# Kernel optimization log

Measured on AMD Instinct MI355X. Metric: run time of the kernel, lower is better.

Reference implementation:

```python
import jax, jax.numpy as jnp
import numpy as np

B, N, T, ET = 256, 256, 100, 4
MSG_HID, MSG_OUT, N_HID, N_CLASSES = 128, 64, 64, 2
N_EDGES = N * (N - 1) // 2  # 32640


def _xavier(k, out_dim, in_dim):
    std = (2.0 / (in_dim + out_dim)) ** 0.5
    return jax.random.normal(k, (out_dim, in_dim), dtype=jnp.float32) * std


def setup_inputs() -> dict:
    key = jax.random.key(0)
    ks = jax.random.split(key, 7)
    return {
        "inputs": jax.random.normal(ks[0], (B, N, T), dtype=jnp.float32),
        "sparse_edges": jax.random.uniform(ks[1], (B, N_EDGES, ET), dtype=jnp.float32),
        "w1": _xavier(ks[2], MSG_HID, N), "b1": jnp.full((MSG_HID,), 0.1, jnp.float32),
        "w2": _xavier(ks[3], MSG_OUT, MSG_HID), "b2": jnp.full((MSG_OUT,), 0.1, jnp.float32),
        "wo1": _xavier(ks[4], N_HID, MSG_OUT), "bo1": jnp.full((N_HID,), 0.1, jnp.float32),
        "wo2": _xavier(ks[5], N_HID, N_HID), "bo2": jnp.full((N_HID,), 0.1, jnp.float32),
        "wo3": _xavier(ks[6], N_CLASSES, N_HID), "bo3": jnp.full((N_CLASSES,), 0.1, jnp.float32),
    }


def reference(inputs, sparse_edges, w1, b1, w2, b2, wo1, bo1, wo2, bo2, wo3, bo3):
    b, n, _ = inputs.shape
    r, c = np.triu_indices(n, k=1)  # static index pattern
    # Scatter all non-null edge types at once: [B, ET-1, N, N]
    se = jnp.swapaxes(sparse_edges[:, :, 1:], 1, 2)  # [B, ET-1, E]
    adj = jnp.zeros((b, se.shape[1], n, n), dtype=se.dtype)
    adj = adj.at[:, :, r, c].set(se)
    adj = adj + jnp.swapaxes(adj, -1, -2)  # symmetrize
    # Message MLP (dropout_prob = 0 -> identity)
    h = jax.nn.relu(jnp.einsum('beij,hj->beih', adj, w1) + b1)   # [B,ET-1,N,msg_hid]
    m = jax.nn.relu(jnp.einsum('beih,oh->beio', h, w2) + b2)     # [B,ET-1,N,msg_out]
    # Weighted sum over edge types: weight for type i is i*0.2, i=1..ET-1
    wts = (jnp.arange(1, sparse_edges.shape[2]) * 0.2).astype(m.dtype)
    out = jnp.einsum('beio,e->bio', m, wts)                      # [B,N,msg_out]
    # Output head
    p = jax.nn.relu(out @ wo1.T + bo1)
    p = jax.nn.relu(p @ wo2.T + bo2)
    p = jnp.mean(p, axis=1)  # mean over atoms
    return p @ wo3.T + bo3   # [B, n_classes]
```

## Files before the change

### kernel.cpp

```cpp
#include <hip/hip_runtime.h>

#define E_ 32640

typedef __bf16 bf16x8 __attribute__((ext_vector_type(8)));
typedef float f32x4 __attribute__((ext_vector_type(4)));

__device__ __forceinline__ unsigned short cvt1(float f) {
  return __builtin_bit_cast(unsigned short, (__bf16)f);
}

__device__ __forceinline__ bf16x8 ldfrag(const unsigned short* base, int row, int kbyte, int rowbytes) {
  int byte = (row * rowbytes + kbyte) ^ ((row & 7) << 4);
  return *reinterpret_cast<const bf16x8*>(reinterpret_cast<const char*>(base) + byte);
}
__device__ __forceinline__ void st2(unsigned short* base, int row, int colbyte, int rowbytes, unsigned short v) {
  int byte = (row * rowbytes + colbyte) ^ ((row & 7) << 4);
  *reinterpret_cast<unsigned short*>(reinterpret_cast<char*>(base) + byte) = v;
}
__device__ __forceinline__ void stA3(unsigned short* sA0, int lr, int cb, float4 v) {
  int byte = (lr * 512 + cb) ^ ((lr & 7) << 4);
  char* p = reinterpret_cast<char*>(sA0) + byte;
  *reinterpret_cast<unsigned short*>(p)         = cvt1(v.y);
  *reinterpret_cast<unsigned short*>(p + 8192)  = cvt1(v.z);
  *reinterpret_cast<unsigned short*>(p + 16384) = cvt1(v.w);
}
__device__ __forceinline__ bf16x8 pack8(float4 lo, float4 hi) {
  bf16x8 r;
  r[0] = (__bf16)lo.x; r[1] = (__bf16)lo.y; r[2] = (__bf16)lo.z; r[3] = (__bf16)lo.w;
  r[4] = (__bf16)hi.x; r[5] = (__bf16)hi.y; r[6] = (__bf16)hi.z; r[7] = (__bf16)hi.w;
  return r;
}

__device__ __forceinline__ int ubase(int i) { return (i * (511 - i)) >> 1; }

__device__ __forceinline__ void decode_g(int g, int& gi, int& j) {
  float disc = (float)(261121 - 8 * g);
  int t = (int)((511.0f - sqrtf(disc)) * 0.5f);
  while (t * (511 - t) > 2 * g) --t;
  while ((t + 1) * (510 - t) <= 2 * g) ++t;
  gi = t;
  j = g - ((t * (511 - t)) >> 1) + t + 1;
}

__device__ __forceinline__ void stage_lower(const float4* seB, unsigned short* sA,
                                            int r0, int glane, int ngroups) {
  const int sub = glane >> 4, l16 = glane & 15;
  const int nStrips = r0 + 15;
  for (int j0 = sub; j0 < nStrips; j0 += ngroups * 4) {
    float4 v[4]; int lr[4], cb[4]; bool ok[4];
    #pragma unroll
    for (int kk = 0; kk < 4; ++kk) {
      int j  = j0 + kk * ngroups;
      int i0 = (j + 1 > r0) ? (j + 1) : r0;
      int cnt = r0 + 16 - i0;
      int ii = i0 + l16;
      bool val = (j < nStrips) && (l16 < cnt);
      int u = j * 255 - ((j * (j - 1)) >> 1) + (ii - j - 1);
      ok[kk] = val; lr[kk] = ii - r0; cb[kk] = j * 2;
      v[kk] = seB[val ? u : 0];
    }
    #pragma unroll
    for (int kk = 0; kk < 4; ++kk)
      if (ok[kk]) stA3(sA, lr[kk], cb[kk], v[kk]);
  }
}

__device__ __forceinline__ void stage_upper_sync(const float4* seB, unsigned short* sA,
                                                 int r0, int tid) {
  const int s0 = ubase(r0);
  const int S  = ubase(r0 + 16) - s0;
  int t = tid;
  float4 p0 = {}, p1 = {};
  if (t < S)       p0 = seB[s0 + t];
  if (t + 512 < S) p1 = seB[s0 + t + 512];
  for (; t < S; t += 512) {
    float4 v = p0; p0 = p1;
    if (t + 1024 < S) p1 = seB[s0 + t + 1024];
    int gi, j; decode_g(s0 + t, gi, j);
    stA3(sA, gi - r0, j * 2, v);
  }
}

__global__ __launch_bounds__(512, 2) void chunk_kernel(
    const float* __restrict__ se_g,
    const float* __restrict__ w1,  const float* __restrict__ b1,
    const float* __restrict__ w2,  const float* __restrict__ b2,
    const float* __restrict__ wo1, const float* __restrict__ bo1,
    const float* __restrict__ wo2, const float* __restrict__ bo2,
    float* __restrict__ ws)
{
  __shared__ __align__(16) unsigned short sA[3 * 16 * 256];
  __shared__ __align__(16) unsigned short sH3[3 * 16 * 128];
  __shared__ __align__(16) unsigned short sXP[2 * 16 * 64];
  __shared__ float sAccC[64];

  const int tid = threadIdx.x;
  const int i   = blockIdx.x;
  const int half  = i >> 8;
  const int within = i & 255;
  const int batch = (within & 7) * 32 + (within >> 3);
  const int cbase = half * 8;

  const int w   = tid >> 6;
  const int l   = tid & 63;
  const int l15 = l & 15;
  const int lk  = l >> 4;
  const int kb0 = lk * 16;

  const int c1 = w;
  const int c2 = w & 3;
  const bool isHead = (w < 4);

  if (tid < 64) sAccC[tid] = 0.f;

  bf16x8 W1f[8];
  {
    const float* p = w1 + (c1 * 16 + l15) * 256 + lk * 8;
    #pragma unroll
    for (int ks = 0; ks < 8; ++ks)
      W1f[ks] = pack8(*reinterpret_cast<const float4*>(p + ks * 32),
                      *reinterpret_cast<const float4*>(p + ks * 32 + 4));
  }
  bf16x8 W2f[4];
  {
    const float* p = w2 + (c2 * 16 + l15) * 128 + lk * 8;
    #pragma unroll
    for (int ks = 0; ks < 4; ++ks)
      W2f[ks] = pack8(*reinterpret_cast<const float4*>(p + ks * 32),
                      *reinterpret_cast<const float4*>(p + ks * 32 + 4));
  }
  const float b1v  = b1[c1 * 16 + l15];
  const float b2v  = b2[c2 * 16 + l15];
  const float bo1v = bo1[c2 * 16 + l15];
  const float bo2v = bo2[c2 * 16 + l15];

  const float4* seB = reinterpret_cast<const float4*>(se_g) + (size_t)batch * E_;
  unsigned short* sX = sXP;
  unsigned short* sP = sXP + 16 * 64;

  {
    int r0 = cbase * 16;
    stage_upper_sync(seB, sA, r0, tid);
    stage_lower(seB, sA, r0, tid, 32);
    if (tid < 16) {
      int byte = (tid * 512 + (r0 + tid) * 2) ^ ((tid & 7) << 4);
      char* p = reinterpret_cast<char*>(sA) + byte;
      *reinterpret_cast<unsigned short*>(p)         = 0;
      *reinterpret_cast<unsigned short*>(p + 8192)  = 0;
      *reinterpret_cast<unsigned short*>(p + 16384) = 0;
    }
  }
  __syncthreads();

  for (int cc = 0; cc < 8; ++cc) {
    const int r0 = (cbase + cc) * 16;
    const bool more = (cc < 7);
    const int nr0 = r0 + 16;

    float4 pf[8];
    int s0 = 0, S = 0;
    if (more) {
      s0 = ubase(nr0);
      S  = ubase(nr0 + 16) - s0;
      #pragma unroll
      for (int k = 0; k < 8; ++k) {
        int t = tid + k * 512;
        pf[k] = seB[s0 + (t < S ? t : 0)];
      }
    }

    {
      const int ccol = c1 * 16 + l15;
      #pragma unroll
      for (int e = 0; e < 3; ++e) {
        f32x4 acc = {0, 0, 0, 0};
        const unsigned short* sAe = sA + e * 4096;
        #pragma unroll
        for (int ks = 0; ks < 8; ++ks)
          acc = __builtin_amdgcn_mfma_f32_16x16x32_bf16(
              ldfrag(sAe, l15, ks * 64 + kb0, 512), W1f[ks], acc, 0, 0, 0);
        unsigned short* sHe = sH3 + e * 2048;
        #pragma unroll
        for (int r = 0; r < 4; ++r)
          st2(sHe, lk * 4 + r, ccol * 2, 256, cvt1(fmaxf(acc[r] + b1v, 0.f)));
      }
    }
    __syncthreads();

    if (more) {
      #pragma unroll
      for (int k = 0; k < 8; ++k) {
        int t = tid + k * 512;
        if (t < S) {
          int gi, j; decode_g(s0 + t, gi, j);
          stA3(sA, gi - nr0, j * 2, pf[k]);
        }
      }
      if (tid < 16) {
        int byte = (tid * 512 + (nr0 + tid) * 2) ^ ((tid & 7) << 4);
        char* p = reinterpret_cast<char*>(sA) + byte;
        *reinterpret_cast<unsigned short*>(p)         = 0;
        *reinterpret_cast<unsigned short*>(p + 8192)  = 0;
        *reinterpret_cast<unsigned short*>(p + 16384) = 0;
      }
    }
    bf16x8 WO1f[2], WO2f[2];
    if (isHead) {
      const float* q1 = wo1 + (c2 * 16 + l15) * 64 + lk * 8;
      const float* q2 = wo2 + (c2 * 16 + l15) * 64 + lk * 8;
      float4 wa0 = *reinterpret_cast<const float4*>(q1);
      float4 wa1 = *reinterpret_cast<const float4*>(q1 + 4);
      float4 wa2 = *reinterpret_cast<const float4*>(q1 + 32);
      float4 wa3 = *reinterpret_cast<const float4*>(q1 + 36);
      float4 wb0 = *reinterpret_cast<const float4*>(q2);
      float4 wb1 = *reinterpret_cast<const float4*>(q2 + 4);
      float4 wb2 = *reinterpret_cast<const float4*>(q2 + 32);
      float4 wb3 = *reinterpret_cast<const float4*>(q2 + 36);
      f32x4 outAcc = {0, 0, 0, 0};
      #pragma unroll
      for (int e = 0; e < 3; ++e) {
        f32x4 acc = {0, 0, 0, 0};
        const unsigned short* sHe = sH3 + e * 2048;
        #pragma unroll
        for (int ks = 0; ks < 4; ++ks)
          acc = __builtin_amdgcn_mfma_f32_16x16x32_bf16(
              ldfrag(sHe, l15, ks * 64 + kb0, 256), W2f[ks], acc, 0, 0, 0);
        float wte = 0.2f * (float)(e + 1);
        #pragma unroll
        for (int r = 0; r < 4; ++r)
          outAcc[r] += wte * fmaxf(acc[r] + b2v, 0.f);
      }
      WO1f[0] = pack8(wa0, wa1); WO1f[1] = pack8(wa2, wa3);
      WO2f[0] = pack8(wb0, wb1); WO2f[1] = pack8(wb2, wb3);
      #pragma unroll
      for (int r = 0; r < 4; ++r)
        st2(sX, lk * 4 + r, (c2 * 16 + l15) * 2, 128, cvt1(outAcc[r]));
    } else if (more) {
      stage_lower(seB, sA, nr0, tid - 256, 16);
    }
    __syncthreads();

    if (isHead) {
      f32x4 acc = {0, 0, 0, 0};
      #pragma unroll
      for (int ks = 0; ks < 2; ++ks)
        acc = __builtin_amdgcn_mfma_f32_16x16x32_bf16(
            ldfrag(sX, l15, ks * 64 + kb0, 128), WO1f[ks], acc, 0, 0, 0);
      #pragma unroll
      for (int r = 0; r < 4; ++r)
        st2(sP, lk * 4 + r, (c2 * 16 + l15) * 2, 128, cvt1(fmaxf(acc[r] + bo1v, 0.f)));
    }
    __syncthreads();

    if (isHead) {
      f32x4 acc = {0, 0, 0, 0};
      #pragma unroll
      for (int ks = 0; ks < 2; ++ks)
        acc = __builtin_amdgcn_mfma_f32_16x16x32_bf16(
            ldfrag(sP, l15, ks * 64 + kb0, 128), WO2f[ks], acc, 0, 0, 0);
      float s = 0.f;
      #pragma unroll
      for (int r = 0; r < 4; ++r) s += fmaxf(acc[r] + bo2v, 0.f);
      s += __shfl_xor(s, 16);
      s += __shfl_xor(s, 32);
      if (lk == 0) sAccC[c2 * 16 + l15] += s;
    }
    __syncthreads();
  }

  if (tid < 64) ws[((size_t)batch * 2 + half) * 64 + tid] = sAccC[tid];
}

__global__ __launch_bounds__(512) void finish_kernel(
    const float* __restrict__ ws,
    const float* __restrict__ wo3, const float* __restrict__ bo3,
    float* __restrict__ out)
{
  int b = blockIdx.x * 8 + (threadIdx.x >> 6);
  int l = threadIdx.x & 63;
  float s = (ws[((size_t)b * 2 + 0) * 64 + l] + ws[((size_t)b * 2 + 1) * 64 + l]) * (1.0f / 256.0f);
  float v0 = s * wo3[l];
  float v1 = s * wo3[64 + l];
  #pragma unroll
  for (int off = 32; off > 0; off >>= 1) {
    v0 += __shfl_down(v0, off);
    v1 += __shfl_down(v1, off);
  }
  if (l == 0) {
    out[b * 2 + 0] = v0 + bo3[0];
    out[b * 2 + 1] = v1 + bo3[1];
  }
}

extern "C" void kernel_launch(void* const* d_in, const int* in_sizes, int n_in,
                              void* d_out, int out_size, void* d_ws, size_t ws_size,
                              hipStream_t stream) {
  (void)in_sizes; (void)n_in; (void)ws_size; (void)out_size;
  const float* se  = (const float*)d_in[1];
  const float* w1  = (const float*)d_in[2];
  const float* b1  = (const float*)d_in[3];
  const float* w2  = (const float*)d_in[4];
  const float* b2  = (const float*)d_in[5];
  const float* wo1 = (const float*)d_in[6];
  const float* bo1 = (const float*)d_in[7];
  const float* wo2 = (const float*)d_in[8];
  const float* bo2 = (const float*)d_in[9];
  const float* wo3 = (const float*)d_in[10];
  const float* bo3 = (const float*)d_in[11];
  float* ws = (float*)d_ws;
  chunk_kernel<<<dim3(512), dim3(512), 0, stream>>>(
      se, w1, b1, w2, b2, wo1, bo1, wo2, bo2, ws);
  finish_kernel<<<dim3(32), dim3(512), 0, stream>>>(ws, wo3, bo3, (float*)d_out);
}
```

Baseline: 103.8 us.

## Split into densify pass writing bf16 adjacency to workspace, then async-DMA GEMM kernel

Adds a densify kernel that scatters the sparse edge list into dense bf16 adjacency planes in global workspace. A separate GEMM kernel then streams 32-row tiles through double-buffered LDS via global_load_lds. It processes 32 rows per MFMA pass and keeps all head weights in registers. The aim is to take the irregular scatter and triangular index decoding off the MFMA critical path and to overlap loads with compute. The cost is about 100MB of extra global write and read traffic plus an extra launch. The old fused kernel stays as a fallback when the workspace is too small.

```diff
diff --git a/kernel.cpp b/kernel.cpp
--- a/kernel.cpp
+++ b/kernel.cpp
@@ -1,6 +1,9 @@
 #include <hip/hip_runtime.h>
 
 #define E_ 32640
+#define PLANE_B 131072ull
+#define AG_BYTES (256ull * 3ull * PLANE_B)
+#define WS_NEED (AG_BYTES + 512ull * 64ull * 4ull)
 
 typedef __bf16 bf16x8 __attribute__((ext_vector_type(8)));
 typedef float f32x4 __attribute__((ext_vector_type(4)));
@@ -16,13 +19,6 @@
 __device__ __forceinline__ void st2(unsigned short* base, int row, int colbyte, int rowbytes, unsigned short v) {
   int byte = (row * rowbytes + colbyte) ^ ((row & 7) << 4);
   *reinterpret_cast<unsigned short*>(reinterpret_cast<char*>(base) + byte) = v;
-}
-__device__ __forceinline__ void stA3(unsigned short* sA0, int lr, int cb, float4 v) {
-  int byte = (lr * 512 + cb) ^ ((lr & 7) << 4);
-  char* p = reinterpret_cast<char*>(sA0) + byte;
-  *reinterpret_cast<unsigned short*>(p)         = cvt1(v.y);
-  *reinterpret_cast<unsigned short*>(p + 8192)  = cvt1(v.z);
-  *reinterpret_cast<unsigned short*>(p + 16384) = cvt1(v.w);
 }
 __device__ __forceinline__ bf16x8 pack8(float4 lo, float4 hi) {
   bf16x8 r;
@@ -30,9 +26,7 @@
   r[4] = (__bf16)hi.x; r[5] = (__bf16)hi.y; r[6] = (__bf16)hi.z; r[7] = (__bf16)hi.w;
   return r;
 }
-
 __device__ __forceinline__ int ubase(int i) { return (i * (511 - i)) >> 1; }
-
 __device__ __forceinline__ void decode_g(int g, int& gi, int& j) {
   float disc = (float)(261121 - 8 * g);
   int t = (int)((511.0f - sqrtf(disc)) * 0.5f);
@@ -42,8 +36,278 @@
   j = g - ((t * (511 - t)) >> 1) + t + 1;
 }
 
-__device__ __forceinline__ void stage_lower(const float4* seB, unsigned short* sA,
-                                            int r0, int glane, int ngroups) {
+__device__ __forceinline__ void stA3_32(unsigned short* sA0, int lr, int cb, float4 v) {
+  int byte = (lr * 512 + cb) ^ ((lr & 7) << 4);
+  char* p = reinterpret_cast<char*>(sA0) + byte;
+  *reinterpret_cast<unsigned short*>(p)         = cvt1(v.y);
+  *reinterpret_cast<unsigned short*>(p + 16384) = cvt1(v.z);
+  *reinterpret_cast<unsigned short*>(p + 32768) = cvt1(v.w);
+}
+__device__ __forceinline__ void stA3_16(unsigned short* sA0, int lr, int cb, float4 v) {
+  int byte = (lr * 512 + cb) ^ ((lr & 7) << 4);
+  char* p = reinterpret_cast<char*>(sA0) + byte;
+  *reinterpret_cast<unsigned short*>(p)         = cvt1(v.y);
+  *reinterpret_cast<unsigned short*>(p + 8192)  = cvt1(v.z);
+  *reinterpret_cast<unsigned short*>(p + 16384) = cvt1(v.w);
+}
+
+#define WAITVM0 asm volatile("s_waitcnt vmcnt(0)" ::: "memory")
+
+__device__ __forceinline__ void gld_lds16(const void* g, void* l) {
+  __builtin_amdgcn_global_load_lds(
+      (const __attribute__((address_space(1))) unsigned int*)g,
+      (__attribute__((address_space(3))) unsigned int*)l, 16, 0, 0);
+}
+__device__ __forceinline__ void dma_tile(const char* g, unsigned short* lbuf, int w, int l) {
+  char* lb = reinterpret_cast<char*>(lbuf);
+  #pragma unroll
+  for (int p = 0; p < 2; ++p) {
+    int seg = (w * 2 + p) * 1024;
+    gld_lds16(g + seg + l * 16, lb + seg);
+  }
+}
+
+__global__ __launch_bounds__(512) void densify_kernel(
+    const float* __restrict__ se_g, char* __restrict__ Ag)
+{
+  __shared__ __align__(16) unsigned short sA[3 * 32 * 256];
+  const int tid = threadIdx.x;
+  const int i = blockIdx.x;
+  const int batch  = (i & 7) * 32 + ((i >> 3) & 31);
+  const int r0     = (i >> 8) * 32;
+  const float4* seB = reinterpret_cast<const float4*>(se_g) + (size_t)batch * E_;
+
+  {
+    const int s0 = ubase(r0);
+    const int S  = ubase(r0 + 32) - s0;
+    int t = tid;
+    float4 p0 = {}, p1 = {};
+    if (t < S)       p0 = seB[s0 + t];
+    if (t + 512 < S) p1 = seB[s0 + t + 512];
+    for (; t < S; t += 512) {
+      float4 v = p0; p0 = p1;
+      if (t + 1024 < S) p1 = seB[s0 + t + 1024];
+      int gi, j; decode_g(s0 + t, gi, j);
+      stA3_32(sA, gi - r0, j * 2, v);
+    }
+  }
+  {
+    const int sub = tid >> 5, l32 = tid & 31;
+    const int K = (r0 + 31 + 15) >> 4;
+    for (int k0 = 0; k0 < K; k0 += 4) {
+      float4 v[4]; int lr[4], cb[4]; bool ok[4];
+      #pragma unroll
+      for (int kk = 0; kk < 4; ++kk) {
+        int j  = sub + ((k0 + kk) << 4);
+        int i0 = (j + 1 > r0) ? (j + 1) : r0;
+        int cnt = r0 + 32 - i0;
+        int ii = i0 + l32;
+        bool val = (j < r0 + 31) && (l32 < cnt);
+        int u = j * 255 - ((j * (j - 1)) >> 1) + (ii - j - 1);
+        ok[kk] = val; lr[kk] = ii - r0; cb[kk] = j * 2;
+        v[kk] = seB[val ? u : 0];
+      }
+      #pragma unroll
+      for (int kk = 0; kk < 4; ++kk)
+        if (ok[kk]) stA3_32(sA, lr[kk], cb[kk], v[kk]);
+    }
+  }
+  if (tid < 32) {
+    int byte = (tid * 512 + (r0 + tid) * 2) ^ ((tid & 7) << 4);
+    char* p = reinterpret_cast<char*>(sA) + byte;
+    *reinterpret_cast<unsigned short*>(p)         = 0;
+    *reinterpret_cast<unsigned short*>(p + 16384) = 0;
+    *reinterpret_cast<unsigned short*>(p + 32768) = 0;
+  }
+  __syncthreads();
+
+  for (int t = tid; t < 3072; t += 512) {
+    int e = t >> 10;
+    int off = (t & 1023) << 4;
+    uint4 v = *reinterpret_cast<const uint4*>(reinterpret_cast<const char*>(sA) + e * 16384 + off);
+    *reinterpret_cast<uint4*>(Ag + ((size_t)(batch * 3 + e)) * PLANE_B + (size_t)r0 * 512 + off) = v;
+  }
+}
+
+__global__ __launch_bounds__(512, 2) void gemm_kernel(
+    const char* __restrict__ Ag,
+    const float* __restrict__ w1,  const float* __restrict__ b1,
+    const float* __restrict__ w2,  const float* __restrict__ b2,
+    const float* __restrict__ wo1, const float* __restrict__ bo1,
+    const float* __restrict__ wo2, const float* __restrict__ bo2,
+    float* __restrict__ pw)
+{
+  __shared__ __align__(16) unsigned short sA2[2 * 32 * 256];
+  __shared__ __align__(16) unsigned short sH3[3 * 32 * 128];
+  __shared__ float sAccW[8][64];
+
+  const int tid = threadIdx.x;
+  const int i = blockIdx.x;
+  const int batch = (i & 7) * 32 + ((i >> 3) & 31);
+  const int half  = i >> 8;
+
+  const int w   = tid >> 6;
+  const int l   = tid & 63;
+  const int l15 = l & 15;
+  const int lk  = l >> 4;
+  const int kb0 = lk * 16;
+  const int c1 = w;
+  const int r2 = w >> 2;
+  const int c2 = w & 3;
+
+  reinterpret_cast<float*>(sAccW)[tid] = 0.f;
+
+  bf16x8 W1f[8];
+  {
+    const float* p = w1 + (c1 * 16 + l15) * 256 + lk * 8;
+    #pragma unroll
+    for (int ks = 0; ks < 8; ++ks)
+      W1f[ks] = pack8(*reinterpret_cast<const float4*>(p + ks * 32),
+                      *reinterpret_cast<const float4*>(p + ks * 32 + 4));
+  }
+  bf16x8 W2f[4];
+  {
+    const float* p = w2 + (c2 * 16 + l15) * 128 + lk * 8;
+    #pragma unroll
+    for (int ks = 0; ks < 4; ++ks)
+      W2f[ks] = pack8(*reinterpret_cast<const float4*>(p + ks * 32),
+                      *reinterpret_cast<const float4*>(p + ks * 32 + 4));
+  }
+  bf16x8 WO1f[2], WO2f[2];
+  {
+    const float* q1 = wo1 + (c2 * 16 + l15) * 64 + lk * 8;
+    const float* q2 = wo2 + (c2 * 16 + l15) * 64 + lk * 8;
+    #pragma unroll
+    for (int ks = 0; ks < 2; ++ks) {
+      WO1f[ks] = pack8(*reinterpret_cast<const float4*>(q1 + ks * 32),
+                       *reinterpret_cast<const float4*>(q1 + ks * 32 + 4));
+      WO2f[ks] = pack8(*reinterpret_cast<const float4*>(q2 + ks * 32),
+                       *reinterpret_cast<const float4*>(q2 + ks * 32 + 4));
+    }
+  }
+  const float b1v  = b1[c1 * 16 + l15];
+  const float b2v  = b2[c2 * 16 + l15];
+  const float bo1v = bo1[c2 * 16 + l15];
+  const float bo2v = bo2[c2 * 16 + l15];
+
+  const char* Abase = Ag + (size_t)batch * 3 * PLANE_B + (size_t)half * 128 * 512;
+  unsigned short* sX = sH3;
+  unsigned short* sP = sH3 + 2048;
+
+  #define TILE_SRC(t) (Abase + (size_t)((t) - ((t) / 3) * 3) * PLANE_B + (size_t)((t) / 3) * 32 * 512)
+
+  dma_tile(TILE_SRC(0), sA2, w, l);
+
+  #pragma unroll 1
+  for (int t = 0; t < 12; ++t) {
+    WAITVM0;
+    __syncthreads();
+    if (t < 11) dma_tile(TILE_SRC(t + 1), sA2 + ((t + 1) & 1) * 8192, w, l);
+
+    {
+      const unsigned short* sAe = sA2 + (t & 1) * 8192;
+      const int e = t - (t / 3) * 3;
+      unsigned short* sHe = sH3 + e * 4096;
+      f32x4 acc0 = {0, 0, 0, 0}, acc1 = {0, 0, 0, 0};
+      #pragma unroll
+      for (int ks = 0; ks < 8; ++ks) {
+        int kb = ks * 64 + kb0;
+        acc0 = __builtin_amdgcn_mfma_f32_16x16x32_bf16(ldfrag(sAe, l15,      kb, 512), W1f[ks], acc0, 0, 0, 0);
+        acc1 = __builtin_amdgcn_mfma_f32_16x16x32_bf16(ldfrag(sAe, 16 + l15, kb, 512), W1f[ks], acc1, 0, 0, 0);
+      }
+      int cc = c1 * 16 + l15;
+      #pragma unroll
+      for (int r = 0; r < 4; ++r) {
+        st2(sHe, lk * 4 + r,      cc * 2, 256, cvt1(fmaxf(acc0[r] + b1v, 0.f)));
+        st2(sHe, 16 + lk * 4 + r, cc * 2, 256, cvt1(fmaxf(acc1[r] + b1v, 0.f)));
+      }
+    }
+
+    if (t - (t / 3) * 3 == 2) {
+      __syncthreads();
+      f32x4 outAcc = {0, 0, 0, 0};
+      {
+        int arow = r2 * 16 + l15;
+        #pragma unroll
+        for (int e = 0; e < 3; ++e) {
+          f32x4 acc = {0, 0, 0, 0};
+          const unsigned short* sHe = sH3 + e * 4096;
+          #pragma unroll
+          for (int ks = 0; ks < 4; ++ks)
+            acc = __builtin_amdgcn_mfma_f32_16x16x32_bf16(
+                ldfrag(sHe, arow, ks * 64 + kb0, 256), W2f[ks], acc, 0, 0, 0);
+          float wte = 0.2f * (float)(e + 1);
+          #pragma unroll
+          for (int r = 0; r < 4; ++r)
+            outAcc[r] += wte * fmaxf(acc[r] + b2v, 0.f);
+        }
+      }
+      __syncthreads();
+      #pragma unroll
+      for (int r = 0; r < 4; ++r)
+        st2(sX, r2 * 16 + lk * 4 + r, (c2 * 16 + l15) * 2, 128, cvt1(outAcc[r]));
+      __syncthreads();
+      {
+        f32x4 acc = {0, 0, 0, 0};
+        int arow = r2 * 16 + l15;
+        #pragma unroll
+        for (int ks = 0; ks < 2; ++ks)
+          acc = __builtin_amdgcn_mfma_f32_16x16x32_bf16(
+              ldfrag(sX, arow, ks * 64 + kb0, 128), WO1f[ks], acc, 0, 0, 0);
+        #pragma unroll
+        for (int r = 0; r < 4; ++r)
+          st2(sP, r2 * 16 + lk * 4 + r, (c2 * 16 + l15) * 2, 128, cvt1(fmaxf(acc[r] + bo1v, 0.f)));
+      }
+      __syncthreads();
+      {
+        f32x4 acc = {0, 0, 0, 0};
+        int arow = r2 * 16 + l15;
+        #pragma unroll
+        for (int ks = 0; ks < 2; ++ks)
+          acc = __builtin_amdgcn_mfma_f32_16x16x32_bf16(
+              ldfrag(sP, arow, ks * 64 + kb0, 128), WO2f[ks], acc, 0, 0, 0);
+        float s = 0.f;
+        #pragma unroll
+        for (int r = 0; r < 4; ++r) s += fmaxf(acc[r] + bo2v, 0.f);
+        s += __shfl_xor(s, 16);
+        s += __shfl_xor(s, 32);
+        if (lk == 0) sAccW[w][c2 * 16 + l15] += s;
+      }
+    }
+  }
+  #undef TILE_SRC
+  __syncthreads();
+  if (tid < 64) {
+    float s = 0.f;
+    #pragma unroll
+    for (int ww = 0; ww < 8; ++ww) s += sAccW[ww][tid];
+    pw[((size_t)batch * 2 + half) * 64 + tid] = s;
+  }
+}
+
+__global__ __launch_bounds__(512) void finish_kernel(
+    const float* __restrict__ pw,
+    const float* __restrict__ wo3, const float* __restrict__ bo3,
+    float* __restrict__ out)
+{
+  int b = blockIdx.x * 8 + (threadIdx.x >> 6);
+  int l = threadIdx.x & 63;
+  float s = (pw[((size_t)b * 2 + 0) * 64 + l] + pw[((size_t)b * 2 + 1) * 64 + l]) * (1.0f / 256.0f);
+  float v0 = s * wo3[l];
+  float v1 = s * wo3[64 + l];
+  #pragma unroll
+  for (int off = 32; off > 0; off >>= 1) {
+    v0 += __shfl_down(v0, off);
+    v1 += __shfl_down(v1, off);
+  }
+  if (l == 0) {
+    out[b * 2 + 0] = v0 + bo3[0];
+    out[b * 2 + 1] = v1 + bo3[1];
+  }
+}
+
+__device__ __forceinline__ void fb_stage_lower(const float4* seB, unsigned short* sA,
+                                               int r0, int glane, int ngroups) {
   const int sub = glane >> 4, l16 = glane & 15;
   const int nStrips = r0 + 15;
   for (int j0 = sub; j0 < nStrips; j0 += ngroups * 4) {
@@ -61,12 +325,11 @@
     }
     #pragma unroll
     for (int kk = 0; kk < 4; ++kk)
-      if (ok[kk]) stA3(sA, lr[kk], cb[kk], v[kk]);
-  }
-}
-
-__device__ __forceinline__ void stage_upper_sync(const float4* seB, unsigned short* sA,
-                                                 int r0, int tid) {
+      if (ok[kk]) stA3_16(sA, lr[kk], cb[kk], v[kk]);
+  }
+}
+__device__ __forceinline__ void fb_stage_upper(const float4* seB, unsigned short* sA,
+                                               int r0, int tid) {
   const int s0 = ubase(r0);
   const int S  = ubase(r0 + 16) - s0;
   int t = tid;
@@ -77,11 +340,11 @@
     float4 v = p0; p0 = p1;
     if (t + 1024 < S) p1 = seB[s0 + t + 1024];
     int gi, j; decode_g(s0 + t, gi, j);
-    stA3(sA, gi - r0, j * 2, v);
-  }
-}
-
-__global__ __launch_bounds__(512, 2) void chunk_kernel(
+    stA3_16(sA, gi - r0, j * 2, v);
+  }
+}
+
+__global__ __launch_bounds__(512, 2) void fb_kernel(
     const float* __restrict__ se_g,
     const float* __restrict__ w1,  const float* __restrict__ b1,
     const float* __restrict__ w2,  const float* __restrict__ b2,
@@ -106,7 +369,6 @@
   const int l15 = l & 15;
   const int lk  = l >> 4;
   const int kb0 = lk * 16;
-
   const int c1 = w;
   const int c2 = w & 3;
   const bool isHead = (w < 4);
@@ -140,8 +402,8 @@
 
   {
     int r0 = cbase * 16;
-    stage_upper_sync(seB, sA, r0, tid);
-    stage_lower(seB, sA, r0, tid, 32);
+    fb_stage_upper(seB, sA, r0, tid);
+    fb_stage_lower(seB, sA, r0, tid, 32);
     if (tid < 16) {
       int byte = (tid * 512 + (r0 + tid) * 2) ^ ((tid & 7) << 4);
       char* p = reinterpret_cast<char*>(sA) + byte;
@@ -168,7 +430,6 @@
         pf[k] = seB[s0 + (t < S ? t : 0)];
       }
     }
-
     {
       const int ccol = c1 * 16 + l15;
       #pragma unroll
@@ -193,7 +454,7 @@
         int t = tid + k * 512;
         if (t < S) {
           int gi, j; decode_g(s0 + t, gi, j);
-          stA3(sA, gi - nr0, j * 2, pf[k]);
+          stA3_16(sA, gi - nr0, j * 2, pf[k]);
         }
       }
       if (tid < 16) {
@@ -208,14 +469,6 @@
     if (isHead) {
       const float* q1 = wo1 + (c2 * 16 + l15) * 64 + lk * 8;
       const float* q2 = wo2 + (c2 * 16 + l15) * 64 + lk * 8;
-      float4 wa0 = *reinterpret_cast<const float4*>(q1);
-      float4 wa1 = *reinterpret_cast<const float4*>(q1 + 4);
-      float4 wa2 = *reinterpret_cast<const float4*>(q1 + 32);
-      float4 wa3 = *reinterpret_cast<const float4*>(q1 + 36);
-      float4 wb0 = *reinterpret_cast<const float4*>(q2);
-      float4 wb1 = *reinterpret_cast<const float4*>(q2 + 4);
-      float4 wb2 = *reinterpret_cast<const float4*>(q2 + 32);
-      float4 wb3 = *reinterpret_cast<const float4*>(q2 + 36);
       f32x4 outAcc = {0, 0, 0, 0};
       #pragma unroll
       for (int e = 0; e < 3; ++e) {
@@ -230,13 +483,15 @@
         for (int r = 0; r < 4; ++r)
           outAcc[r] += wte * fmaxf(acc[r] + b2v, 0.f);
       }
-      WO1f[0] = pack8(wa0, wa1); WO1f[1] = pack8(wa2, wa3);
-      WO2f[0] = pack8(wb0, wb1); WO2f[1] = pack8(wb2, wb3);
+      WO1f[0] = pack8(*reinterpret_cast<const float4*>(q1), *reinterpret_cast<const float4*>(q1 + 4));
+      WO1f[1] = pack8(*reinterpret_cast<const float4*>(q1 + 32), *reinterpret_cast<const float4*>(q1 + 36));
+      WO2f[0] = pack8(*reinterpret_cast<const float4*>(q2), *reinterpret_cast<const float4*>(q2 + 4));
+      WO2f[1] = pack8(*reinterpret_cast<const float4*>(q2 + 32), *reinterpret_cast<const float4*>(q2 + 36));
       #pragma unroll
       for (int r = 0; r < 4; ++r)
         st2(sX, lk * 4 + r, (c2 * 16 + l15) * 2, 128, cvt1(outAcc[r]));
     } else if (more) {
-      stage_lower(seB, sA, nr0, tid - 256, 16);
+      fb_stage_lower(seB, sA, nr0, tid - 256, 16);
     }
     __syncthreads();
 
@@ -251,7 +506,6 @@
         st2(sP, lk * 4 + r, (c2 * 16 + l15) * 2, 128, cvt1(fmaxf(acc[r] + bo1v, 0.f)));
     }
     __syncthreads();
-
     if (isHead) {
       f32x4 acc = {0, 0, 0, 0};
       #pragma unroll
@@ -267,35 +521,13 @@
     }
     __syncthreads();
   }
-
   if (tid < 64) ws[((size_t)batch * 2 + half) * 64 + tid] = sAccC[tid];
-}
-
-__global__ __launch_bounds__(512) void finish_kernel(
-    const float* __restrict__ ws,
-    const float* __restrict__ wo3, const float* __restrict__ bo3,
-    float* __restrict__ out)
-{
-  int b = blockIdx.x * 8 + (threadIdx.x >> 6);
-  int l = threadIdx.x & 63;
-  float s = (ws[((size_t)b * 2 + 0) * 64 + l] + ws[((size_t)b * 2 + 1) * 64 + l]) * (1.0f / 256.0f);
-  float v0 = s * wo3[l];
-  float v1 = s * wo3[64 + l];
-  #pragma unroll
-  for (int off = 32; off > 0; off >>= 1) {
-    v0 += __shfl_down(v0, off);
-    v1 += __shfl_down(v1, off);
-  }
-  if (l == 0) {
-    out[b * 2 + 0] = v0 + bo3[0];
-    out[b * 2 + 1] = v1 + bo3[1];
-  }
 }
 
 extern "C" void kernel_launch(void* const* d_in, const int* in_sizes, int n_in,
                               void* d_out, int out_size, void* d_ws, size_t ws_size,
                               hipStream_t stream) {
-  (void)in_sizes; (void)n_in; (void)ws_size; (void)out_size;
+  (void)in_sizes; (void)n_in; (void)out_size;
   const float* se  = (const float*)d_in[1];
   const float* w1  = (const float*)d_in[2];
   const float* b1  = (const float*)d_in[3];
@@ -307,8 +539,18 @@
   const float* bo2 = (const float*)d_in[9];
   const float* wo3 = (const float*)d_in[10];
   const float* bo3 = (const float*)d_in[11];
-  float* ws = (float*)d_ws;
-  chunk_kernel<<<dim3(512), dim3(512), 0, stream>>>(
-      se, w1, b1, w2, b2, wo1, bo1, wo2, bo2, ws);
-  finish_kernel<<<dim3(32), dim3(512), 0, stream>>>(ws, wo3, bo3, (float*)d_out);
-}
+
+  if (ws_size >= WS_NEED) {
+    char*  Ag = (char*)d_ws;
+    float* pw = (float*)((char*)d_ws + AG_BYTES);
+    densify_kernel<<<dim3(2048), dim3(512), 0, stream>>>(se, Ag);
+    gemm_kernel<<<dim3(512), dim3(512), 0, stream>>>(
+        Ag, w1, b1, w2, b2, wo1, bo1, wo2, bo2, pw);
+    finish_kernel<<<dim3(32), dim3(512), 0, stream>>>(pw, wo3, bo3, (float*)d_out);
+  } else {
+    float* pw = (float*)d_ws;
+    fb_kernel<<<dim3(512), dim3(512), 0, stream>>>(
+        se, w1, b1, w2, b2, wo1, bo1, wo2, bo2, pw);
+    finish_kernel<<<dim3(32), dim3(512), 0, stream>>>(pw, wo3, bo3, (float*)d_out);
+  }
+}
```

Result: slower. 112.3 us (+8.2%).

## Split into per-stripe message kernel and separate per-batch head kernel

Applied to the files above, without the earlier changes.

Replaces the 512-block persistent chunk loop with 4096 independent blocks, one per (batch, 16-row stripe), each staging its adjacency rows and running both message MLP layers, then writing fp32 messages to a workspace. A new head kernel per batch runs the output MLP in 32-row chunks, takes the mean and applies the final projection, so the finish kernel is no longer needed. The lower-triangle staging now reuses upper-triangle loads mirrored within the diagonal block plus contiguous 8-element column loads. This trades the cross-iteration prefetch pipeline for more parallelism and occupancy, at the cost of a 16 MB workspace round trip and redundant weight loading per block.

```diff
diff --git a/kernel.cpp b/kernel.cpp
--- a/kernel.cpp
+++ b/kernel.cpp
@@ -16,13 +16,6 @@
 __device__ __forceinline__ void st2(unsigned short* base, int row, int colbyte, int rowbytes, unsigned short v) {
   int byte = (row * rowbytes + colbyte) ^ ((row & 7) << 4);
   *reinterpret_cast<unsigned short*>(reinterpret_cast<char*>(base) + byte) = v;
-}
-__device__ __forceinline__ void stA3(unsigned short* sA0, int lr, int cb, float4 v) {
-  int byte = (lr * 512 + cb) ^ ((lr & 7) << 4);
-  char* p = reinterpret_cast<char*>(sA0) + byte;
-  *reinterpret_cast<unsigned short*>(p)         = cvt1(v.y);
-  *reinterpret_cast<unsigned short*>(p + 8192)  = cvt1(v.z);
-  *reinterpret_cast<unsigned short*>(p + 16384) = cvt1(v.w);
 }
 __device__ __forceinline__ bf16x8 pack8(float4 lo, float4 hi) {
   bf16x8 r;
@@ -30,9 +23,7 @@
   r[4] = (__bf16)hi.x; r[5] = (__bf16)hi.y; r[6] = (__bf16)hi.z; r[7] = (__bf16)hi.w;
   return r;
 }
-
 __device__ __forceinline__ int ubase(int i) { return (i * (511 - i)) >> 1; }
-
 __device__ __forceinline__ void decode_g(int g, int& gi, int& j) {
   float disc = (float)(261121 - 8 * g);
   int t = (int)((511.0f - sqrtf(disc)) * 0.5f);
@@ -41,65 +32,28 @@
   gi = t;
   j = g - ((t * (511 - t)) >> 1) + t + 1;
 }
-
-__device__ __forceinline__ void stage_lower(const float4* seB, unsigned short* sA,
-                                            int r0, int glane, int ngroups) {
-  const int sub = glane >> 4, l16 = glane & 15;
-  const int nStrips = r0 + 15;
-  for (int j0 = sub; j0 < nStrips; j0 += ngroups * 4) {
-    float4 v[4]; int lr[4], cb[4]; bool ok[4];
-    #pragma unroll
-    for (int kk = 0; kk < 4; ++kk) {
-      int j  = j0 + kk * ngroups;
-      int i0 = (j + 1 > r0) ? (j + 1) : r0;
-      int cnt = r0 + 16 - i0;
-      int ii = i0 + l16;
-      bool val = (j < nStrips) && (l16 < cnt);
-      int u = j * 255 - ((j * (j - 1)) >> 1) + (ii - j - 1);
-      ok[kk] = val; lr[kk] = ii - r0; cb[kk] = j * 2;
-      v[kk] = seB[val ? u : 0];
-    }
-    #pragma unroll
-    for (int kk = 0; kk < 4; ++kk)
-      if (ok[kk]) stA3(sA, lr[kk], cb[kk], v[kk]);
-  }
-}
-
-__device__ __forceinline__ void stage_upper_sync(const float4* seB, unsigned short* sA,
-                                                 int r0, int tid) {
-  const int s0 = ubase(r0);
-  const int S  = ubase(r0 + 16) - s0;
-  int t = tid;
-  float4 p0 = {}, p1 = {};
-  if (t < S)       p0 = seB[s0 + t];
-  if (t + 512 < S) p1 = seB[s0 + t + 512];
-  for (; t < S; t += 512) {
-    float4 v = p0; p0 = p1;
-    if (t + 1024 < S) p1 = seB[s0 + t + 1024];
-    int gi, j; decode_g(s0 + t, gi, j);
-    stA3(sA, gi - r0, j * 2, v);
-  }
-}
-
-__global__ __launch_bounds__(512, 2) void chunk_kernel(
+__device__ __forceinline__ void stA3(unsigned short* sA0, int lr, int cb, float4 v) {
+  int byte = (lr * 512 + cb) ^ ((lr & 7) << 4);
+  char* p = reinterpret_cast<char*>(sA0) + byte;
+  *reinterpret_cast<unsigned short*>(p)         = cvt1(v.y);
+  *reinterpret_cast<unsigned short*>(p + 8192)  = cvt1(v.z);
+  *reinterpret_cast<unsigned short*>(p + 16384) = cvt1(v.w);
+}
+
+__global__ __launch_bounds__(512, 4) void stage1_kernel(
     const float* __restrict__ se_g,
     const float* __restrict__ w1,  const float* __restrict__ b1,
     const float* __restrict__ w2,  const float* __restrict__ b2,
-    const float* __restrict__ wo1, const float* __restrict__ bo1,
-    const float* __restrict__ wo2, const float* __restrict__ bo2,
-    float* __restrict__ ws)
+    float* __restrict__ Mg)
 {
   __shared__ __align__(16) unsigned short sA[3 * 16 * 256];
   __shared__ __align__(16) unsigned short sH3[3 * 16 * 128];
-  __shared__ __align__(16) unsigned short sXP[2 * 16 * 64];
-  __shared__ float sAccC[64];
 
   const int tid = threadIdx.x;
   const int i   = blockIdx.x;
-  const int half  = i >> 8;
-  const int within = i & 255;
-  const int batch = (within & 7) * 32 + (within >> 3);
-  const int cbase = half * 8;
+  const int batch  = (i & 7) * 32 + ((i >> 3) & 31);
+  const int stripe = i >> 8;
+  const int r0     = stripe * 16;
 
   const int w   = tid >> 6;
   const int l   = tid & 63;
@@ -107,188 +61,204 @@
   const int lk  = l >> 4;
   const int kb0 = lk * 16;
 
-  const int c1 = w;
-  const int c2 = w & 3;
-  const bool isHead = (w < 4);
-
-  if (tid < 64) sAccC[tid] = 0.f;
+  const float4* seB = reinterpret_cast<const float4*>(se_g) + (size_t)batch * E_;
+
+  float4 lv[8];
+  const bool hasL = tid < 2 * r0;
+  const int  j_l  = tid >> 1;
+  const int  h_l  = tid & 1;
+  if (hasL) {
+    int u = j_l * 255 - ((j_l * (j_l - 1)) >> 1) + (r0 - j_l - 1) + 8 * h_l;
+    #pragma unroll
+    for (int k = 0; k < 8; ++k) lv[k] = seB[u + k];
+  }
+  const int s0 = ubase(r0);
+  const int S  = ubase(r0 + 16) - s0;
+  float4 pf[8];
+  #pragma unroll
+  for (int k = 0; k < 8; ++k) {
+    int t = tid + k * 512;
+    pf[k] = seB[s0 + (t < S ? t : 0)];
+  }
+
+  if (hasL) {
+    #pragma unroll
+    for (int k = 0; k < 8; ++k)
+      stA3(sA, 8 * h_l + k, j_l * 2, lv[k]);
+  }
+  #pragma unroll
+  for (int k = 0; k < 8; ++k) {
+    int t = tid + k * 512;
+    if (t < S) {
+      int gi, j; decode_g(s0 + t, gi, j);
+      stA3(sA, gi - r0, j * 2, pf[k]);
+      if (j < r0 + 16) stA3(sA, j - r0, gi * 2, pf[k]);
+    }
+  }
+  if (tid < 16) {
+    int byte = (tid * 512 + (r0 + tid) * 2) ^ ((tid & 7) << 4);
+    char* p = reinterpret_cast<char*>(sA) + byte;
+    *reinterpret_cast<unsigned short*>(p)         = 0;
+    *reinterpret_cast<unsigned short*>(p + 8192)  = 0;
+    *reinterpret_cast<unsigned short*>(p + 16384) = 0;
+  }
+  __syncthreads();
 
   bf16x8 W1f[8];
   {
-    const float* p = w1 + (c1 * 16 + l15) * 256 + lk * 8;
+    const float* p = w1 + (w * 16 + l15) * 256 + lk * 8;
     #pragma unroll
     for (int ks = 0; ks < 8; ++ks)
       W1f[ks] = pack8(*reinterpret_cast<const float4*>(p + ks * 32),
                       *reinterpret_cast<const float4*>(p + ks * 32 + 4));
   }
-  bf16x8 W2f[4];
+  const float b1v = b1[w * 16 + l15];
+
+  #pragma unroll
+  for (int e = 0; e < 3; ++e) {
+    f32x4 acc = {0, 0, 0, 0};
+    const unsigned short* sAe = sA + e * 4096;
+    #pragma unroll
+    for (int ks = 0; ks < 8; ++ks)
+      acc = __builtin_amdgcn_mfma_f32_16x16x32_bf16(
+          ldfrag(sAe, l15, ks * 64 + kb0, 512), W1f[ks], acc, 0, 0, 0);
+    unsigned short* sHe = sH3 + e * 2048;
+    int cc = w * 16 + l15;
+    #pragma unroll
+    for (int r = 0; r < 4; ++r)
+      st2(sHe, lk * 4 + r, cc * 2, 256, cvt1(fmaxf(acc[r] + b1v, 0.f)));
+  }
+  __syncthreads();
+
+  if (w < 4) {
+    bf16x8 W2f[4];
+    {
+      const float* p = w2 + (w * 16 + l15) * 128 + lk * 8;
+      #pragma unroll
+      for (int ks = 0; ks < 4; ++ks)
+        W2f[ks] = pack8(*reinterpret_cast<const float4*>(p + ks * 32),
+                        *reinterpret_cast<const float4*>(p + ks * 32 + 4));
+    }
+    const float b2v = b2[w * 16 + l15];
+    f32x4 osum = {0, 0, 0, 0};
+    #pragma unroll
+    for (int e = 0; e < 3; ++e) {
+      f32x4 acc = {0, 0, 0, 0};
+      const unsigned short* sHe = sH3 + e * 2048;
+      #pragma unroll
+      for (int ks = 0; ks < 4; ++ks)
+        acc = __builtin_amdgcn_mfma_f32_16x16x32_bf16(
+            ldfrag(sHe, l15, ks * 64 + kb0, 256), W2f[ks], acc, 0, 0, 0);
+      float wte = 0.2f * (float)(e + 1);
+      #pragma unroll
+      for (int r = 0; r < 4; ++r)
+        osum[r] += wte * fmaxf(acc[r] + b2v, 0.f);
+    }
+    #pragma unroll
+    for (int r = 0; r < 4; ++r)
+      Mg[((size_t)batch * 256 + r0 + lk * 4 + r) * 64 + w * 16 + l15] = osum[r];
+  }
+}
+
+__global__ __launch_bounds__(512) void head_kernel(
+    const float* __restrict__ Mg,
+    const float* __restrict__ wo1, const float* __restrict__ bo1,
+    const float* __restrict__ wo2, const float* __restrict__ bo2,
+    const float* __restrict__ wo3, const float* __restrict__ bo3,
+    float* __restrict__ out)
+{
+  __shared__ __align__(16) unsigned short sX[32 * 64];
+  __shared__ __align__(16) unsigned short sP[32 * 64];
+  __shared__ float sAccW[8][64];
+  __shared__ float sMean[64];
+
+  const int tid = threadIdx.x;
+  const int b   = blockIdx.x;
+  const int w   = tid >> 6;
+  const int l   = tid & 63;
+  const int l15 = l & 15;
+  const int lk  = l >> 4;
+  const int kb0 = lk * 16;
+  const int r2  = w >> 2;
+  const int c2  = w & 3;
+
+  reinterpret_cast<float*>(sAccW)[tid] = 0.f;
+
+  bf16x8 WO1f[2], WO2f[2];
   {
-    const float* p = w2 + (c2 * 16 + l15) * 128 + lk * 8;
-    #pragma unroll
-    for (int ks = 0; ks < 4; ++ks)
-      W2f[ks] = pack8(*reinterpret_cast<const float4*>(p + ks * 32),
-                      *reinterpret_cast<const float4*>(p + ks * 32 + 4));
-  }
-  const float b1v  = b1[c1 * 16 + l15];
-  const float b2v  = b2[c2 * 16 + l15];
+    const float* q1 = wo1 + (c2 * 16 + l15) * 64 + lk * 8;
+    const float* q2 = wo2 + (c2 * 16 + l15) * 64 + lk * 8;
+    #pragma unroll
+    for (int ks = 0; ks < 2; ++ks) {
+      WO1f[ks] = pack8(*reinterpret_cast<const float4*>(q1 + ks * 32),
+                       *reinterpret_cast<const float4*>(q1 + ks * 32 + 4));
+      WO2f[ks] = pack8(*reinterpret_cast<const float4*>(q2 + ks * 32),
+                       *reinterpret_cast<const float4*>(q2 + ks * 32 + 4));
+    }
+  }
   const float bo1v = bo1[c2 * 16 + l15];
   const float bo2v = bo2[c2 * 16 + l15];
 
-  const float4* seB = reinterpret_cast<const float4*>(se_g) + (size_t)batch * E_;
-  unsigned short* sX = sXP;
-  unsigned short* sP = sXP + 16 * 64;
-
-  {
-    int r0 = cbase * 16;
-    stage_upper_sync(seB, sA, r0, tid);
-    stage_lower(seB, sA, r0, tid, 32);
-    if (tid < 16) {
-      int byte = (tid * 512 + (r0 + tid) * 2) ^ ((tid & 7) << 4);
-      char* p = reinterpret_cast<char*>(sA) + byte;
-      *reinterpret_cast<unsigned short*>(p)         = 0;
-      *reinterpret_cast<unsigned short*>(p + 8192)  = 0;
-      *reinterpret_cast<unsigned short*>(p + 16384) = 0;
-    }
-  }
-  __syncthreads();
-
-  for (int cc = 0; cc < 8; ++cc) {
-    const int r0 = (cbase + cc) * 16;
-    const bool more = (cc < 7);
-    const int nr0 = r0 + 16;
-
-    float4 pf[8];
-    int s0 = 0, S = 0;
-    if (more) {
-      s0 = ubase(nr0);
-      S  = ubase(nr0 + 16) - s0;
-      #pragma unroll
-      for (int k = 0; k < 8; ++k) {
-        int t = tid + k * 512;
-        pf[k] = seB[s0 + (t < S ? t : 0)];
-      }
-    }
-
-    {
-      const int ccol = c1 * 16 + l15;
-      #pragma unroll
-      for (int e = 0; e < 3; ++e) {
-        f32x4 acc = {0, 0, 0, 0};
-        const unsigned short* sAe = sA + e * 4096;
-        #pragma unroll
-        for (int ks = 0; ks < 8; ++ks)
-          acc = __builtin_amdgcn_mfma_f32_16x16x32_bf16(
-              ldfrag(sAe, l15, ks * 64 + kb0, 512), W1f[ks], acc, 0, 0, 0);
-        unsigned short* sHe = sH3 + e * 2048;
-        #pragma unroll
-        for (int r = 0; r < 4; ++r)
-          st2(sHe, lk * 4 + r, ccol * 2, 256, cvt1(fmaxf(acc[r] + b1v, 0.f)));
-      }
+  const int xr = tid >> 4;
+  const int xc = (tid & 15) * 4;
+  const float* Mb = Mg + (size_t)b * 256 * 64;
+
+  float4 nv = *reinterpret_cast<const float4*>(Mb + xr * 64 + xc);
+
+  for (int ch = 0; ch < 8; ++ch) {
+    {
+      unsigned p01 = ((unsigned)cvt1(nv.y) << 16) | cvt1(nv.x);
+      unsigned p23 = ((unsigned)cvt1(nv.w) << 16) | cvt1(nv.z);
+      int byte = (xr * 128 + xc * 2) ^ ((xr & 7) << 4);
+      uint2 u = make_uint2(p01, p23);
+      *reinterpret_cast<uint2*>(reinterpret_cast<char*>(sX) + byte) = u;
     }
     __syncthreads();
-
-    if (more) {
-      #pragma unroll
-      for (int k = 0; k < 8; ++k) {
-        int t = tid + k * 512;
-        if (t < S) {
-          int gi, j; decode_g(s0 + t, gi, j);
-          stA3(sA, gi - nr0, j * 2, pf[k]);
-        }
-      }
-      if (tid < 16) {
-        int byte = (tid * 512 + (nr0 + tid) * 2) ^ ((tid & 7) << 4);
-        char* p = reinterpret_cast<char*>(sA) + byte;
-        *reinterpret_cast<unsigned short*>(p)         = 0;
-        *reinterpret_cast<unsigned short*>(p + 8192)  = 0;
-        *reinterpret_cast<unsigned short*>(p + 16384) = 0;
-      }
-    }
-    bf16x8 WO1f[2], WO2f[2];
-    if (isHead) {
-      const float* q1 = wo1 + (c2 * 16 + l15) * 64 + lk * 8;
-      const float* q2 = wo2 + (c2 * 16 + l15) * 64 + lk * 8;
-      float4 wa0 = *reinterpret_cast<const float4*>(q1);
-      float4 wa1 = *reinterpret_cast<const float4*>(q1 + 4);
-      float4 wa2 = *reinterpret_cast<const float4*>(q1 + 32);
-      float4 wa3 = *reinterpret_cast<const float4*>(q1 + 36);
-      float4 wb0 = *reinterpret_cast<const float4*>(q2);
-      float4 wb1 = *reinterpret_cast<const float4*>(q2 + 4);
-      float4 wb2 = *reinterpret_cast<const float4*>(q2 + 32);
-      float4 wb3 = *reinterpret_cast<const float4*>(q2 + 36);
-      f32x4 outAcc = {0, 0, 0, 0};
-      #pragma unroll
-      for (int e = 0; e < 3; ++e) {
-        f32x4 acc = {0, 0, 0, 0};
-        const unsigned short* sHe = sH3 + e * 2048;
-        #pragma unroll
-        for (int ks = 0; ks < 4; ++ks)
-          acc = __builtin_amdgcn_mfma_f32_16x16x32_bf16(
-              ldfrag(sHe, l15, ks * 64 + kb0, 256), W2f[ks], acc, 0, 0, 0);
-        float wte = 0.2f * (float)(e + 1);
-        #pragma unroll
-        for (int r = 0; r < 4; ++r)
-          outAcc[r] += wte * fmaxf(acc[r] + b2v, 0.f);
-      }
-      WO1f[0] = pack8(wa0, wa1); WO1f[1] = pack8(wa2, wa3);
-      WO2f[0] = pack8(wb0, wb1); WO2f[1] = pack8(wb2, wb3);
-      #pragma unroll
-      for (int r = 0; r < 4; ++r)
-        st2(sX, lk * 4 + r, (c2 * 16 + l15) * 2, 128, cvt1(outAcc[r]));
-    } else if (more) {
-      stage_lower(seB, sA, nr0, tid - 256, 16);
-    }
-    __syncthreads();
-
-    if (isHead) {
+    if (ch < 7)
+      nv = *reinterpret_cast<const float4*>(Mb + ((ch + 1) * 32 + xr) * 64 + xc);
+
+    {
       f32x4 acc = {0, 0, 0, 0};
+      int arow = r2 * 16 + l15;
       #pragma unroll
       for (int ks = 0; ks < 2; ++ks)
         acc = __builtin_amdgcn_mfma_f32_16x16x32_bf16(
-            ldfrag(sX, l15, ks * 64 + kb0, 128), WO1f[ks], acc, 0, 0, 0);
+            ldfrag(sX, arow, ks * 64 + kb0, 128), WO1f[ks], acc, 0, 0, 0);
       #pragma unroll
       for (int r = 0; r < 4; ++r)
-        st2(sP, lk * 4 + r, (c2 * 16 + l15) * 2, 128, cvt1(fmaxf(acc[r] + bo1v, 0.f)));
+        st2(sP, r2 * 16 + lk * 4 + r, (c2 * 16 + l15) * 2, 128, cvt1(fmaxf(acc[r] + bo1v, 0.f)));
     }
     __syncthreads();
-
-    if (isHead) {
+    {
       f32x4 acc = {0, 0, 0, 0};
+      int arow = r2 * 16 + l15;
       #pragma unroll
       for (int ks = 0; ks < 2; ++ks)
         acc = __builtin_amdgcn_mfma_f32_16x16x32_bf16(
-            ldfrag(sP, l15, ks * 64 + kb0, 128), WO2f[ks], acc, 0, 0, 0);
+            ldfrag(sP, arow, ks * 64 + kb0, 128), WO2f[ks], acc, 0, 0, 0);
       float s = 0.f;
       #pragma unroll
       for (int r = 0; r < 4; ++r) s += fmaxf(acc[r] + bo2v, 0.f);
       s += __shfl_xor(s, 16);
       s += __shfl_xor(s, 32);
-      if (lk == 0) sAccC[c2 * 16 + l15] += s;
+      if (lk == 0) sAccW[w][c2 * 16 + l15] += s;
     }
     __syncthreads();
   }
 
-  if (tid < 64) ws[((size_t)batch * 2 + half) * 64 + tid] = sAccC[tid];
-}
-
-__global__ __launch_bounds__(512) void finish_kernel(
-    const float* __restrict__ ws,
-    const float* __restrict__ wo3, const float* __restrict__ bo3,
-    float* __restrict__ out)
-{
-  int b = blockIdx.x * 8 + (threadIdx.x >> 6);
-  int l = threadIdx.x & 63;
-  float s = (ws[((size_t)b * 2 + 0) * 64 + l] + ws[((size_t)b * 2 + 1) * 64 + l]) * (1.0f / 256.0f);
-  float v0 = s * wo3[l];
-  float v1 = s * wo3[64 + l];
-  #pragma unroll
-  for (int off = 32; off > 0; off >>= 1) {
-    v0 += __shfl_down(v0, off);
-    v1 += __shfl_down(v1, off);
-  }
-  if (l == 0) {
-    out[b * 2 + 0] = v0 + bo3[0];
-    out[b * 2 + 1] = v1 + bo3[1];
+  if (tid < 64) {
+    float s = 0.f;
+    #pragma unroll
+    for (int ww = 0; ww < 8; ++ww) s += sAccW[ww][tid];
+    sMean[tid] = s * (1.0f / 256.0f);
+  }
+  __syncthreads();
+  if (tid < 128) {
+    int c = tid >> 6;
+    float v = sMean[l] * wo3[c * 64 + l];
+    #pragma unroll
+    for (int off = 32; off > 0; off >>= 1) v += __shfl_down(v, off);
+    if (l == 0) out[b * 2 + c] = v + bo3[c];
   }
 }
 
@@ -307,8 +277,8 @@
   const float* bo2 = (const float*)d_in[9];
   const float* wo3 = (const float*)d_in[10];
   const float* bo3 = (const float*)d_in[11];
-  float* ws = (float*)d_ws;
-  chunk_kernel<<<dim3(512), dim3(512), 0, stream>>>(
-      se, w1, b1, w2, b2, wo1, bo1, wo2, bo2, ws);
-  finish_kernel<<<dim3(32), dim3(512), 0, stream>>>(ws, wo3, bo3, (float*)d_out);
-}
+
+  float* Mg = (float*)d_ws;
+  stage1_kernel<<<dim3(4096), dim3(512), 0, stream>>>(se, w1, b1, w2, b2, Mg);
+  head_kernel<<<dim3(256), dim3(512), 0, stream>>>(Mg, wo1, bo1, wo2, bo2, wo3, bo3, (float*)d_out);
+}
```

New measurement: 111.6 us. 7.5% more time.
